# Kernel optimization log

Hardware: AMD Instinct MI355X
Metric: run time of the kernel (lower is better)

Reference implementation:

```python
import jax, jax.numpy as jnp
import numpy as np
from jax.scipy.special import ndtr

EPS1 = 1e-6
WEIGHT_DECAY = 1e-5  # FLAGS.weight_decay


def setup_inputs() -> dict:
    key = jax.random.key(0)
    ks = jax.random.split(key, 12)
    B, F, C, Z, S = 512, 512, 500, 64, 100  # batch, features, classes (r_dim), z_dim, n_sample
    lim = np.sqrt(6.0 / (C + Z))
    def glorot(k, shape):
        fan_in, fan_out = shape
        s = np.sqrt(2.0 / (fan_in + fan_out))
        return jax.random.normal(k, shape, jnp.float32) * s
    return {
        "input_X": jax.random.normal(ks[0], (B, F), jnp.float32),
        "input_Y": (jax.random.uniform(ks[1], (B, C)) < 0.1).astype(jnp.float32),  # multi-label targets
        "noise": jax.random.normal(ks[2], (S, B, Z), jnp.float32),
        "W1": glorot(ks[3], (F, 128)), "b1": jnp.zeros((128,), jnp.float32),
        "W2": glorot(ks[4], (128, 256)), "b2": jnp.zeros((256,), jnp.float32),
        "W3": glorot(ks[5], (256, 256)), "b3": jnp.zeros((256,), jnp.float32),
        "Wmu": glorot(ks[6], (256, C)), "bmu": jnp.zeros((C,), jnp.float32),
        "r_sqrt_sigma": jax.random.uniform(ks[7], (C, Z), jnp.float32, -lim, lim),
    }


def reference(input_X, input_Y, noise, W1, b1, W2, b2, W3, b3, Wmu, bmu, r_sqrt_sigma):
    # MLP trunk
    h = jax.nn.relu(input_X @ W1 + b1)
    h = jax.nn.relu(h @ W2 + b2)
    feature = jax.nn.relu(h @ W3 + b3)

    # low-rank covariance: sigma = R R^T, covariance = sigma + I
    cov_diag = jnp.sum(r_sqrt_sigma * r_sqrt_sigma, axis=1) + 1.0  # [C]

    normalized_mu = feature @ Wmu + bmu            # [B, C]
    r_mu = normalized_mu * jnp.sqrt(cov_diag)      # [B, C]

    # MC samples of latent r: [S, B, C]
    sample_r = jnp.einsum('sbz,cz->sbc', noise, r_sqrt_sigma) + r_mu

    E = ndtr(sample_r) * (1.0 - EPS1) + EPS1 * 0.5  # probit CDF, clamped
    # logprob = sum_c [ Y*log(E) + (1-Y)*log(1-E) ]  (== -sum sample_nll)
    logprob = jnp.sum(jnp.log(E) * input_Y + jnp.log1p(-E) * (1.0 - input_Y), axis=2)  # [S, B]
    maxlogprob = jnp.max(logprob, axis=0)                       # [B]
    Eprob = jnp.mean(jnp.exp(logprob - maxlogprob), axis=0)     # [B]
    nll_loss = jnp.mean(-jnp.log(Eprob) - maxlogprob)

    # marginal (independent) probit approximated by scaled sigmoid
    indiv_prob = jax.nn.sigmoid(normalized_mu * 1.70169) * (1.0 - EPS1) + 0.5 * EPS1
    cross_entropy = jnp.log(indiv_prob) * input_Y + jnp.log1p(-indiv_prob) * (1.0 - input_Y)
    marginal_loss = -jnp.mean(jnp.sum(cross_entropy, axis=1))

    l2_loss = WEIGHT_DECAY * (jnp.sum(W1 * W1) + jnp.sum(W2 * W2)
                              + jnp.sum(W3 * W3) + jnp.sum(Wmu * Wmu))
    total_loss = l2_loss + nll_loss
    return indiv_prob, nll_loss, marginal_loss, l2_loss, total_loss
```

## Files before the change

### kernel.cpp

```cpp
#include <hip/hip_runtime.h>
#include <cstddef>

#define EPS1f 1e-6f
#define WDf   1e-5f

constexpr int Bsz = 512, Csz = 500, Zsz = 64, Ssz = 100;

typedef short bf16x8 __attribute__((ext_vector_type(8)));
typedef float f32x4 __attribute__((ext_vector_type(4)));

__device__ inline short f2bf(float f) {
  union { float f; unsigned u; } v; v.f = f;
  unsigned r = (v.u + 0x7fffu + ((v.u >> 16) & 1u)) >> 16;
  return (short)r;
}

__device__ inline float block_reduce_sum(float v, float* red) {
  #pragma unroll
  for (int off = 32; off > 0; off >>= 1) v += __shfl_down(v, off, 64);
  const int lane = threadIdx.x & 63, wid = threadIdx.x >> 6;
  if (lane == 0) red[wid] = v;
  __syncthreads();
  float r = 0.f;
  if (threadIdx.x == 0) {
    const int nw = blockDim.x >> 6;
    for (int i = 0; i < nw; ++i) r += red[i];
  }
  __syncthreads();
  return r;
}

__device__ __forceinline__ void gemm32_body(
    const float* __restrict__ A, const float* __restrict__ W,
    const float* __restrict__ bias, float* __restrict__ out,
    int M, int N, int K, int bn0, int bm0, float* As_, float* Ws_, bool relu) {
  const int tid = threadIdx.x;
  const int bn = bn0 * 32, bm = bm0 * 32;
  const int sm = tid >> 3, sk4 = (tid & 7) * 4;
  const int sk = tid >> 3, sn4 = (tid & 7) * 4;
  const int tn = tid & 15, tm = tid >> 4;
  #define AS_(b, k, m) As_[(b) * 1152 + (k) * 36 + (m)]
  #define WS_(b, k, n) Ws_[(b) * 1152 + (k) * 36 + (n)]
  auto loadW = [&](int kt, float4& wv) {
    const float* wrow = W + (size_t)(kt + sk) * N;
    const int nn = bn + sn4;
    if (nn + 3 < N) wv = *reinterpret_cast<const float4*>(wrow + nn);
    else {
      wv.x = (nn + 0 < N) ? wrow[nn + 0] : 0.f;
      wv.y = (nn + 1 < N) ? wrow[nn + 1] : 0.f;
      wv.z = (nn + 2 < N) ? wrow[nn + 2] : 0.f;
      wv.w = (nn + 3 < N) ? wrow[nn + 3] : 0.f;
    }
  };
  {
    float4 av = *reinterpret_cast<const float4*>(A + (size_t)(bm + sm) * K + sk4);
    float4 wv; loadW(0, wv);
    AS_(0, sk4 + 0, sm) = av.x; AS_(0, sk4 + 1, sm) = av.y;
    AS_(0, sk4 + 2, sm) = av.z; AS_(0, sk4 + 3, sm) = av.w;
    *reinterpret_cast<float4*>(&WS_(0, sk, sn4)) = wv;
  }
  __syncthreads();
  float acc[2][2] = {};
  int pb = 0;
  for (int kt = 0; kt < K; kt += 32) {
    const bool more = (kt + 32) < K;
    float4 av2, wv2;
    if (more) {
      av2 = *reinterpret_cast<const float4*>(A + (size_t)(bm + sm) * K + kt + 32 + sk4);
      loadW(kt + 32, wv2);
    }
    #pragma unroll
    for (int k = 0; k < 32; ++k) {
      const float2 a = *reinterpret_cast<const float2*>(&AS_(pb, k, tm * 2));
      const float2 w = *reinterpret_cast<const float2*>(&WS_(pb, k, tn * 2));
      acc[0][0] = fmaf(a.x, w.x, acc[0][0]);
      acc[0][1] = fmaf(a.x, w.y, acc[0][1]);
      acc[1][0] = fmaf(a.y, w.x, acc[1][0]);
      acc[1][1] = fmaf(a.y, w.y, acc[1][1]);
    }
    if (more) {
      const int nb = pb ^ 1;
      AS_(nb, sk4 + 0, sm) = av2.x; AS_(nb, sk4 + 1, sm) = av2.y;
      AS_(nb, sk4 + 2, sm) = av2.z; AS_(nb, sk4 + 3, sm) = av2.w;
      *reinterpret_cast<float4*>(&WS_(nb, sk, sn4)) = wv2;
      __syncthreads();
      pb = nb;
    }
  }
  #pragma unroll
  for (int j = 0; j < 2; ++j) {
    const int n = bn + tn * 2 + j;
    if (n >= N) continue;
    const float bv = bias[n];
    #pragma unroll
    for (int i = 0; i < 2; ++i) {
      const int m = bm + tm * 2 + i;
      float v = acc[i][j] + bv;
      if (relu) v = fmaxf(v, 0.f);
      out[(size_t)m * N + n] = v;
    }
  }
  #undef AS_
  #undef WS_
}

__global__ __launch_bounds__(256) void prep_kernel(
    const float* __restrict__ noise, short* __restrict__ nfB,
    const float* __restrict__ R, short* __restrict__ RbF, float* __restrict__ sqrtcov,
    const float* __restrict__ X, const float* __restrict__ W1,
    const float* __restrict__ b1, float* __restrict__ h1,
    const float* __restrict__ W2, const float* __restrict__ W3,
    const float* __restrict__ Wmu, float* __restrict__ l2_part,
    float* __restrict__ rsP, float* __restrict__ snP) {
  __shared__ float smem[2304 * 2];
  const int blk = blockIdx.x;
  const int tid = threadIdx.x;
  if (blk < 800) {
    const int g = blk * 256 + tid;
    const int s = g >> 11;
    const int r = g & 2047;
    const int bt = r >> 6;
    const int ln = r & 63;
    const int cl = ln & 15, grp = ln >> 4;
    const float* src = noise + ((size_t)(s * 512 + bt * 16 + cl) * 64 + grp * 8);
    const float4 a = *reinterpret_cast<const float4*>(src);
    const float4 b = *reinterpret_cast<const float4*>(src + 4);
    const float4 c = *reinterpret_cast<const float4*>(src + 32);
    const float4 d = *reinterpret_cast<const float4*>(src + 36);
    bf16x8* dst = reinterpret_cast<bf16x8*>(nfB);
    const int u = (s * 32 + bt) * 128 + ln;
    dst[u]      = bf16x8{ f2bf(a.x), f2bf(a.y), f2bf(a.z), f2bf(a.w),
                          f2bf(b.x), f2bf(b.y), f2bf(b.z), f2bf(b.w) };
    dst[u + 64] = bf16x8{ f2bf(c.x), f2bf(c.y), f2bf(c.z), f2bf(c.w),
                          f2bf(d.x), f2bf(d.y), f2bf(d.z), f2bf(d.w) };
  } else if (blk < 808) {
    const int idx = (blk - 800) * 256 + tid;
    const int c = idx >> 2;
    const int zq = (idx & 3) * 16;
    const bool cv = c < Csz;
    const float* src = R + (size_t)c * Zsz + zq;
    float ss = 0.f;
    if (cv) {
      #pragma unroll
      for (int q = 0; q < 4; ++q) {
        const float4 r4 = *reinterpret_cast<const float4*>(src + q * 4);
        ss = fmaf(r4.x, r4.x, ss); ss = fmaf(r4.y, r4.y, ss);
        ss = fmaf(r4.z, r4.z, ss); ss = fmaf(r4.w, r4.w, ss);
      }
    }
    ss += __shfl_xor(ss, 1, 64);
    ss += __shfl_xor(ss, 2, 64);
    if ((idx & 3) == 0 && cv) sqrtcov[c] = sqrtf(1.f + ss);
  } else if (blk < 824) {
    const int e = (blk - 808) * 256 + tid;
    const int ct = e >> 7;
    const int f = (e >> 6) & 1;
    const int lane = e & 63;
    const int cl = lane & 15, grp = lane >> 4;
    const int c = ct * 16 + cl;
    bf16x8 out = {0, 0, 0, 0, 0, 0, 0, 0};
    if (c < Csz) {
      const float* src = R + (size_t)c * Zsz + f * 32 + grp * 8;
      const float4 a = *reinterpret_cast<const float4*>(src);
      const float4 b = *reinterpret_cast<const float4*>(src + 4);
      out = bf16x8{ f2bf(a.x), f2bf(a.y), f2bf(a.z), f2bf(a.w),
                    f2bf(b.x), f2bf(b.y), f2bf(b.z), f2bf(b.w) };
    }
    reinterpret_cast<bf16x8*>(RbF)[e] = out;
  } else if (blk < 888) {
    const int bid = blk - 824;
    const int gid = bid * 256 + tid;
    const int stride = 64 * 256;
    float s = 0.f;
    for (int i = gid; i < 65536; i += stride) { float v = W1[i]; s = fmaf(v, v, s); }
    for (int i = gid; i < 32768; i += stride) { float v = W2[i]; s = fmaf(v, v, s); }
    for (int i = gid; i < 65536; i += stride) { float v = W3[i]; s = fmaf(v, v, s); }
    for (int i = gid; i < 128000; i += stride) { float v = Wmu[i]; s = fmaf(v, v, s); }
    const float tot = block_reduce_sum(s, smem);
    if (tid == 0) l2_part[bid] = tot;
  } else if (blk < 952) {
    const int idx = blk - 888;
    gemm32_body(X, W1, b1, h1, 512, 128, 512, idx & 3, idx >> 2,
                smem, smem + 2304, true);
  } else {
    const int g = (blk - 952) * 256 + tid;
    const int m = g >> 4;
    const int n = 496 + (g & 15);
    const int idx = ((n >> 4) * 32 + (m >> 4)) * 256
                  + (((n >> 2) & 3) * 16 + (m & 15)) * 4 + (n & 3);
    rsP[idx] = 0.f;
    snP[idx] = -0.70710678f;
  }
}

template <bool RELU>
__global__ __launch_bounds__(256) void gemm32(
    const float* __restrict__ A, const float* __restrict__ W,
    const float* __restrict__ bias, float* __restrict__ out,
    int M, int N, int K) {
  __shared__ float smem[2304 * 2];
  gemm32_body(A, W, bias, out, M, N, K, blockIdx.x, blockIdx.y,
              smem, smem + 2304, RELU);
}

__global__ __launch_bounds__(256) void gemm32_mu(
    const float* __restrict__ A, const float* __restrict__ W,
    const float* __restrict__ bias, const float* __restrict__ Y,
    const float* __restrict__ sqrtcov,
    float* __restrict__ out_prob, float* __restrict__ rsP, float* __restrict__ snP,
    float* __restrict__ ce_part, int M, int N, int K) {
  __shared__ float As[2][32][36];
  __shared__ float Ws[2][32][36];
  const int tid = threadIdx.x;
  const int bn = blockIdx.x * 32, bm = blockIdx.y * 32;
  const int sm = tid >> 3, sk4 = (tid & 7) * 4;
  const int sk = tid >> 3, sn4 = (tid & 7) * 4;
  const int tn = tid & 15, tm = tid >> 4;

  auto loadW = [&](int kt, float4& wv) {
    const float* wrow = W + (size_t)(kt + sk) * N;
    const int nn = bn + sn4;
    if (nn + 3 < N) wv = *reinterpret_cast<const float4*>(wrow + nn);
    else {
      wv.x = (nn + 0 < N) ? wrow[nn + 0] : 0.f;
      wv.y = (nn + 1 < N) ? wrow[nn + 1] : 0.f;
      wv.z = (nn + 2 < N) ? wrow[nn + 2] : 0.f;
      wv.w = (nn + 3 < N) ? wrow[nn + 3] : 0.f;
    }
  };
  {
    float4 av = *reinterpret_cast<const float4*>(A + (size_t)(bm + sm) * K + sk4);
    float4 wv; loadW(0, wv);
    As[0][sk4 + 0][sm] = av.x; As[0][sk4 + 1][sm] = av.y;
    As[0][sk4 + 2][sm] = av.z; As[0][sk4 + 3][sm] = av.w;
    *reinterpret_cast<float4*>(&Ws[0][sk][sn4]) = wv;
  }
  __syncthreads();
  float acc[2][2] = {};
  int pb = 0;
  for (int kt = 0; kt < K; kt += 32) {
    const bool more = (kt + 32) < K;
    float4 av2, wv2;
    if (more) {
      av2 = *reinterpret_cast<const float4*>(A + (size_t)(bm + sm) * K + kt + 32 + sk4);
      loadW(kt + 32, wv2);
    }
    #pragma unroll
    for (int k = 0; k < 32; ++k) {
      const float2 a = *reinterpret_cast<const float2*>(&As[pb][k][tm * 2]);
      const float2 w = *reinterpret_cast<const float2*>(&Ws[pb][k][tn * 2]);
      acc[0][0] = fmaf(a.x, w.x, acc[0][0]);
      acc[0][1] = fmaf(a.x, w.y, acc[0][1]);
      acc[1][0] = fmaf(a.y, w.x, acc[1][0]);
      acc[1][1] = fmaf(a.y, w.y, acc[1][1]);
    }
    if (more) {
      const int nb = pb ^ 1;
      As[nb][sk4 + 0][sm] = av2.x; As[nb][sk4 + 1][sm] = av2.y;
      As[nb][sk4 + 2][sm] = av2.z; As[nb][sk4 + 3][sm] = av2.w;
      *reinterpret_cast<float4*>(&Ws[nb][sk][sn4]) = wv2;
      __syncthreads();
      pb = nb;
    }
  }
  float ce2[2] = {0.f, 0.f};
  #pragma unroll
  for (int i = 0; i < 2; ++i) {
    const int m = bm + tm * 2 + i;
    #pragma unroll
    for (int j = 0; j < 2; ++j) {
      const int n = bn + tn * 2 + j;
      if (n < N) {
        const float v = acc[i][j] + bias[n];
        const float sp = __builtin_amdgcn_rcpf(1.f + __expf(-1.70169f * v));
        const float p = fmaf(sp, 1.f - EPS1f, 0.5f * EPS1f);
        const float q = fmaf(1.f - sp, 1.f - EPS1f, 0.5f * EPS1f);
        const float y = Y[(size_t)m * N + n];
        out_prob[(size_t)m * N + n] = p;
        ce2[i] += __logf((y > 0.5f) ? p : q);
        const int idx = (((n >> 4) * 32 + (m >> 4)) << 8)
                      + ((((n >> 2) & 3) * 16 + (m & 15)) << 2) + (n & 3);
        const float snc = (y > 0.5f) ? -0.70710678f : 0.70710678f;
        snP[idx] = snc;
        rsP[idx] = v * sqrtcov[n] * snc;
      }
    }
  }
  #pragma unroll
  for (int off = 1; off < 16; off <<= 1) {
    ce2[0] += __shfl_xor(ce2[0], off, 64);
    ce2[1] += __shfl_xor(ce2[1], off, 64);
  }
  if (tn == 0) {
    const int m0 = bm + tm * 2;
    ce_part[(size_t)blockIdx.x * Bsz + m0] = ce2[0];
    ce_part[(size_t)blockIdx.x * Bsz + m0 + 1] = ce2[1];
  }
}

__global__ void logprob_s3(
    const short* __restrict__ nfB, const short* __restrict__ RbF,
    const float* __restrict__ rsP, const float* __restrict__ snP,
    float* __restrict__ lp4) {
  const int blk = blockIdx.x;
  const int chh = blk & 1;
  const int btg = (blk >> 1) & 15;
  const int s = blk >> 5;
  const int wid = threadIdx.x >> 6;
  const int lane = threadIdx.x & 63;
  const int bt = btg * 2 + (wid & 1);
  const int chq = chh * 2 + (wid >> 1);

  const bf16x8* nf = reinterpret_cast<const bf16x8*>(nfB);
  const int nbase = (s * 32 + bt) * 128 + lane;
  const bf16x8 n0 = nf[nbase];
  const bf16x8 n1 = nf[nbase + 64];
  const bf16x8* rf = reinterpret_cast<const bf16x8*>(RbF);

  float lpl = 0.f;
  #pragma unroll
  for (int t = 0; t < 8; ++t) {
    const int ct = chq * 8 + t;
    const bf16x8 Rf0 = rf[(ct * 2 + 0) * 64 + lane];
    const bf16x8 Rf1 = rf[(ct * 2 + 1) * 64 + lane];
    f32x4 acc = {0.f, 0.f, 0.f, 0.f};
    acc = __builtin_amdgcn_mfma_f32_16x16x32_bf16(Rf0, n0, acc, 0, 0, 0);
    acc = __builtin_amdgcn_mfma_f32_16x16x32_bf16(Rf1, n1, acc, 0, 0, 0);
    const int fb = (ct * 32 + bt) * 256 + lane * 4;
    const float4 rs4 = *reinterpret_cast<const float4*>(rsP + fb);
    const float4 sn4 = *reinterpret_cast<const float4*>(snP + fb);
    float u[4], sc[4], p[4], e[4];
    u[0] = fmaf(acc[0], sn4.x, rs4.x);
    u[1] = fmaf(acc[1], sn4.y, rs4.y);
    u[2] = fmaf(acc[2], sn4.z, rs4.z);
    u[3] = fmaf(acc[3], sn4.w, rs4.w);
    #pragma unroll
    for (int i = 0; i < 4; ++i)
      sc[i] = __builtin_amdgcn_rcpf(fmaf(0.3275911f, fabsf(u[i]), 1.f));
    #pragma unroll
    for (int i = 0; i < 4; ++i) {
      float q = fmaf(0.5307027145f, sc[i], -0.7265760135f);
      q = fmaf(q, sc[i], 0.7107068705f);
      q = fmaf(q, sc[i], -0.142248368f);
      q = fmaf(q, sc[i], 0.127414796f);
      p[i] = q * sc[i];
    }
    #pragma unroll
    for (int i = 0; i < 4; ++i) e[i] = __expf(-u[i] * u[i]);
    #pragma unroll
    for (int i = 0; i < 4; ++i) {
      const float f = p[i] * e[i];
      const float Phi = (u[i] < 0.f) ? 1.f - f : f;
      lpl += __log2f(fmaf(Phi, 1.f - EPS1f, 0.5f * EPS1f));
    }
  }
  lpl += __shfl_xor(lpl, 16, 64);
  lpl += __shfl_xor(lpl, 32, 64);
  if (lane < 16) {
    const float fix = (chq == 3) ? 12.0f : 0.f;
    lp4[(size_t)(chq * Ssz + s) * 512 + bt * 16 + lane] =
        (lpl + fix) * 0.69314718055994531f;
  }
}

__global__ __launch_bounds__(256) void nll_kernel(const float* __restrict__ lp4,
                                                  float* __restrict__ nll_b) {
  __shared__ float sm[4][64], sse[4][64];
  const int bl = threadIdx.x & 63;
  const int sc = threadIdx.x >> 6;
  const int b = blockIdx.x * 64 + bl;
  float m = -3.0e38f, se = 0.f;
  for (int s = sc * 25; s < sc * 25 + 25; ++s) {
    const float v = lp4[(size_t)s * 512 + b]
                  + lp4[(size_t)(Ssz + s) * 512 + b]
                  + lp4[(size_t)(2 * Ssz + s) * 512 + b]
                  + lp4[(size_t)(3 * Ssz + s) * 512 + b];
    const float mn = fmaxf(m, v);
    se = se * __expf(m - mn) + __expf(v - mn);
    m = mn;
  }
  sm[sc][bl] = m; sse[sc][bl] = se;
  __syncthreads();
  if (sc == 0) {
    float M = sm[0][bl];
    #pragma unroll
    for (int i = 1; i < 4; ++i) M = fmaxf(M, sm[i][bl]);
    float SE = 0.f;
    #pragma unroll
    for (int i = 0; i < 4; ++i) SE += sse[i][bl] * __expf(sm[i][bl] - M);
    nll_b[b] = -__logf(SE * (1.f / (float)Ssz)) - M;
  }
}

__global__ __launch_bounds__(256) void finals_kernel(
    const float* __restrict__ nll_b, const float* __restrict__ ce_part,
    const float* __restrict__ l2_part, int nparts, float* __restrict__ out4) {
  __shared__ float red[4];
  const int t = threadIdx.x;
  const float snll = block_reduce_sum(nll_b[t] + nll_b[t + 256], red);
  float ce = 0.f;
  #pragma unroll
  for (int i = 0; i < 32; ++i) ce += ce_part[i * 256 + t];
  const float sce = block_reduce_sum(ce, red);
  const float sl2 = block_reduce_sum((t < nparts) ? l2_part[t] : 0.f, red);
  if (t == 0) {
    const float nll = snll / (float)Bsz;
    const float marg = -sce / (float)Bsz;
    const float l2v = WDf * sl2;
    out4[0] = nll;
    out4[1] = marg;
    out4[2] = l2v;
    out4[3] = l2v + nll;
  }
}

extern "C" void kernel_launch(void* const* d_in, const int* in_sizes, int n_in,
                              void* d_out, int out_size, void* d_ws, size_t ws_size,
                              hipStream_t stream) {
  const float* X = (const float*)d_in[0];
  const float* Y = (const float*)d_in[1];
  const float* noise = (const float*)d_in[2];
  const float* W1 = (const float*)d_in[3];
  const float* b1 = (const float*)d_in[4];
  const float* W2 = (const float*)d_in[5];
  const float* b2 = (const float*)d_in[6];
  const float* W3 = (const float*)d_in[7];
  const float* b3 = (const float*)d_in[8];
  const float* Wmu = (const float*)d_in[9];
  const float* bmu = (const float*)d_in[10];
  const float* rss = (const float*)d_in[11];

  float* ws = (float*)d_ws;
  float* h1 = ws;
  float* h2 = h1 + 65536;
  float* feat = h2 + 131072;
  float* B0 = ws + 327680;
  float* sqrtcov = B0;
  float* rsP = sqrtcov + 512;
  float* snP = rsP + 262144;
  float* ce_part = snP + 262144;
  float* nll_b = ce_part + 8192;
  float* l2_part = nll_b + 512;
  float* lp4 = l2_part + 128;
  short* RbF = (short*)(lp4 + 204800);
  short* nfB = RbF + 32768;

  float* out_prob = (float*)d_out;
  float* out4 = out_prob + (size_t)Bsz * Csz;

  prep_kernel<<<dim3(984), 256, 0, stream>>>(noise, nfB, rss, RbF, sqrtcov,
                                             X, W1, b1, h1, W2, W3, Wmu, l2_part,
                                             rsP, snP);

  gemm32<true><<<dim3(8, 16), 256, 0, stream>>>(h1, W2, b2, h2, 512, 256, 128);
  gemm32<true><<<dim3(8, 16), 256, 0, stream>>>(h2, W3, b3, feat, 512, 256, 256);
  gemm32_mu<<<dim3(16, 16), 256, 0, stream>>>(feat, Wmu, bmu, Y, sqrtcov,
                                              out_prob, rsP, snP, ce_part, 512, 500, 256);

  logprob_s3<<<dim3(3200), 256, 0, stream>>>(nfB, RbF, rsP, snP, lp4);
  nll_kernel<<<dim3(8), 256, 0, stream>>>(lp4, nll_b);

  finals_kernel<<<dim3(1), 256, 0, stream>>>(nll_b, ce_part, l2_part, 64, out4);
}
```

Before: 72.16 us.

## Pack label bit into rs LSB and stage R fragments in LDS

Stores the label sign in the least significant bit of the precomputed scaled-mean float, so the separate sign array is no longer written or read. This halves the per-element side data streamed by the logprob kernel. The logprob kernel is also remapped so each block handles one class quarter across four batch tiles, and it loads the R fragments once into shared memory for all four waves to reuse instead of each wave fetching them from global memory. Forcing the low mantissa bit adds a tiny precision perturbation and one barrier per block.

```diff
diff --git a/kernel.cpp b/kernel.cpp
--- a/kernel.cpp
+++ b/kernel.cpp
@@ -111,7 +111,7 @@
     const float* __restrict__ b1, float* __restrict__ h1,
     const float* __restrict__ W2, const float* __restrict__ W3,
     const float* __restrict__ Wmu, float* __restrict__ l2_part,
-    float* __restrict__ rsP, float* __restrict__ snP) {
+    unsigned* __restrict__ rsPu) {
   __shared__ float smem[2304 * 2];
   const int blk = blockIdx.x;
   const int tid = threadIdx.x;
@@ -188,8 +188,7 @@
     const int n = 496 + (g & 15);
     const int idx = ((n >> 4) * 32 + (m >> 4)) * 256
                   + (((n >> 2) & 3) * 16 + (m & 15)) * 4 + (n & 3);
-    rsP[idx] = 0.f;
-    snP[idx] = -0.70710678f;
+    rsPu[idx] = 0u;
   }
 }
 
@@ -207,7 +206,7 @@
     const float* __restrict__ A, const float* __restrict__ W,
     const float* __restrict__ bias, const float* __restrict__ Y,
     const float* __restrict__ sqrtcov,
-    float* __restrict__ out_prob, float* __restrict__ rsP, float* __restrict__ snP,
+    float* __restrict__ out_prob, unsigned* __restrict__ rsPu,
     float* __restrict__ ce_part, int M, int N, int K) {
   __shared__ float As[2][32][36];
   __shared__ float Ws[2][32][36];
@@ -281,8 +280,9 @@
         const int idx = (((n >> 4) * 32 + (m >> 4)) << 8)
                       + ((((n >> 2) & 3) * 16 + (m & 15)) << 2) + (n & 3);
         const float snc = (y > 0.5f) ? -0.70710678f : 0.70710678f;
-        snP[idx] = snc;
-        rsP[idx] = v * sqrtcov[n] * snc;
+        unsigned bits = __float_as_uint(v * sqrtcov[n] * snc);
+        bits = (bits & ~1u) | ((y > 0.5f) ? 1u : 0u);
+        rsPu[idx] = bits;
       }
     }
   }
@@ -298,42 +298,48 @@
   }
 }
 
-__global__ void logprob_s3(
+__global__ void logprob_s4(
     const short* __restrict__ nfB, const short* __restrict__ RbF,
-    const float* __restrict__ rsP, const float* __restrict__ snP,
-    float* __restrict__ lp4) {
+    const unsigned* __restrict__ rsPu, float* __restrict__ lp4) {
   const int blk = blockIdx.x;
-  const int chh = blk & 1;
-  const int btg = (blk >> 1) & 15;
+  const int chq = blk & 3;
+  const int btg = (blk >> 2) & 7;
   const int s = blk >> 5;
   const int wid = threadIdx.x >> 6;
   const int lane = threadIdx.x & 63;
-  const int bt = btg * 2 + (wid & 1);
-  const int chq = chh * 2 + (wid >> 1);
+  const int bt = btg * 4 + wid;
+
+  __shared__ short lds[16 * 64 * 8];
+  bf16x8* ldsv = reinterpret_cast<bf16x8*>(lds);
+  const bf16x8* rf = reinterpret_cast<const bf16x8*>(RbF);
+  #pragma unroll
+  for (int e = 0; e < 4; ++e)
+    ldsv[(e * 4 + wid) * 64 + lane] = rf[(chq * 16 + e * 4 + wid) * 64 + lane];
 
   const bf16x8* nf = reinterpret_cast<const bf16x8*>(nfB);
   const int nbase = (s * 32 + bt) * 128 + lane;
   const bf16x8 n0 = nf[nbase];
   const bf16x8 n1 = nf[nbase + 64];
-  const bf16x8* rf = reinterpret_cast<const bf16x8*>(RbF);
+  __syncthreads();
 
   float lpl = 0.f;
   #pragma unroll
   for (int t = 0; t < 8; ++t) {
     const int ct = chq * 8 + t;
-    const bf16x8 Rf0 = rf[(ct * 2 + 0) * 64 + lane];
-    const bf16x8 Rf1 = rf[(ct * 2 + 1) * 64 + lane];
+    const bf16x8 Rf0 = ldsv[(t * 2 + 0) * 64 + lane];
+    const bf16x8 Rf1 = ldsv[(t * 2 + 1) * 64 + lane];
     f32x4 acc = {0.f, 0.f, 0.f, 0.f};
     acc = __builtin_amdgcn_mfma_f32_16x16x32_bf16(Rf0, n0, acc, 0, 0, 0);
     acc = __builtin_amdgcn_mfma_f32_16x16x32_bf16(Rf1, n1, acc, 0, 0, 0);
-    const int fb = (ct * 32 + bt) * 256 + lane * 4;
-    const float4 rs4 = *reinterpret_cast<const float4*>(rsP + fb);
-    const float4 sn4 = *reinterpret_cast<const float4*>(snP + fb);
+    const uint4 qv = *reinterpret_cast<const uint4*>(rsPu + (ct * 32 + bt) * 256 + lane * 4);
+    const unsigned qq[4] = {qv.x, qv.y, qv.z, qv.w};
     float u[4], sc[4], p[4], e[4];
-    u[0] = fmaf(acc[0], sn4.x, rs4.x);
-    u[1] = fmaf(acc[1], sn4.y, rs4.y);
-    u[2] = fmaf(acc[2], sn4.z, rs4.z);
-    u[3] = fmaf(acc[3], sn4.w, rs4.w);
+    #pragma unroll
+    for (int i = 0; i < 4; ++i) {
+      const float rs = __uint_as_float(qq[i]);
+      const float sn = __uint_as_float(0x3F3504F3u ^ ((qq[i] & 1u) << 31));
+      u[i] = fmaf(acc[i], sn, rs);
+    }
     #pragma unroll
     for (int i = 0; i < 4; ++i)
       sc[i] = __builtin_amdgcn_rcpf(fmaf(0.3275911f, fabsf(u[i]), 1.f));
@@ -436,9 +442,8 @@
   float* feat = h2 + 131072;
   float* B0 = ws + 327680;
   float* sqrtcov = B0;
-  float* rsP = sqrtcov + 512;
-  float* snP = rsP + 262144;
-  float* ce_part = snP + 262144;
+  unsigned* rsPu = (unsigned*)(sqrtcov + 512);
+  float* ce_part = (float*)(rsPu + 262144);
   float* nll_b = ce_part + 8192;
   float* l2_part = nll_b + 512;
   float* lp4 = l2_part + 128;
@@ -450,14 +455,14 @@
 
   prep_kernel<<<dim3(984), 256, 0, stream>>>(noise, nfB, rss, RbF, sqrtcov,
                                              X, W1, b1, h1, W2, W3, Wmu, l2_part,
-                                             rsP, snP);
+                                             rsPu);
 
   gemm32<true><<<dim3(8, 16), 256, 0, stream>>>(h1, W2, b2, h2, 512, 256, 128);
   gemm32<true><<<dim3(8, 16), 256, 0, stream>>>(h2, W3, b3, feat, 512, 256, 256);
   gemm32_mu<<<dim3(16, 16), 256, 0, stream>>>(feat, Wmu, bmu, Y, sqrtcov,
-                                              out_prob, rsP, snP, ce_part, 512, 500, 256);
-
-  logprob_s3<<<dim3(3200), 256, 0, stream>>>(nfB, RbF, rsP, snP, lp4);
+                                              out_prob, rsPu, ce_part, 512, 500, 256);
+
+  logprob_s4<<<dim3(3200), 256, 0, stream>>>(nfB, RbF, rsPu, lp4);
   nll_kernel<<<dim3(8), 256, 0, stream>>>(lp4, nll_b);
 
   finals_kernel<<<dim3(1), 256, 0, stream>>>(nll_b, ce_part, l2_part, 64, out4);
```

Result: no change. 73.53 us (+1.9%).
